# Kernel tuning notes

Hardware: AMD Instinct MI355X
Metric: run time of the kernel (lower is better)

Reference implementation:

```python
import jax, jax.numpy as jnp
import numpy as np

GROUPS = 32
EPS = 1e-5
HEADS = 8

def setup_inputs() -> dict:
    key = jax.random.key(0)
    ks = jax.random.split(key, 7)
    b, c, H, W = 16, 512, 32, 32
    x = jax.random.normal(ks[0], (b, c, H, W), dtype=jnp.float32)
    gn_scale = jax.random.normal(ks[1], (c,), dtype=jnp.float32) * 0.02 + 1.0
    gn_bias = jax.random.normal(ks[2], (c,), dtype=jnp.float32) * 0.02
    w_qkv = jax.random.normal(ks[3], (3 * c, c), dtype=jnp.float32) / np.sqrt(c)
    b_qkv = jax.random.normal(ks[4], (3 * c,), dtype=jnp.float32) * 0.01
    # original zero-initializes proj_out; use random weights for a non-trivial baseline
    w_proj = jax.random.normal(ks[5], (c, c), dtype=jnp.float32) / np.sqrt(c)
    b_proj = jax.random.normal(ks[6], (c,), dtype=jnp.float32) * 0.01
    return {"x": x, "gn_scale": gn_scale, "gn_bias": gn_bias,
            "w_qkv": w_qkv, "b_qkv": b_qkv, "w_proj": w_proj, "b_proj": b_proj}

def _group_norm(x, scale, bias):
    # x: [b, c, T]; normalize over (c//GROUPS, T) per group
    b, c, T = x.shape
    xg = x.reshape(b, GROUPS, (c // GROUPS) * T)
    mean = xg.mean(axis=-1, keepdims=True)
    var = xg.var(axis=-1, keepdims=True)
    xn = ((xg - mean) * jax.lax.rsqrt(var + EPS)).reshape(b, c, T)
    return xn * scale[None, :, None] + bias[None, :, None]

def reference(x, gn_scale, gn_bias, w_qkv, b_qkv, w_proj, b_proj):
    b, c, H, W = x.shape
    T = H * W
    xf = x.reshape(b, c, T)
    h = _group_norm(xf, gn_scale, gn_bias)
    qkv = jnp.einsum('oc,bct->bot', w_qkv, h) + b_qkv[None, :, None]  # [b, 3c, T]
    qkv = qkv.reshape(b * HEADS, 3 * (c // HEADS), T)
    ch = c // HEADS
    q, k, v = jnp.split(qkv, 3, axis=1)  # each [b*heads, ch, T]
    scale = 1.0 / np.sqrt(np.sqrt(ch))
    weight = jnp.einsum('bct,bcs->bts', q * scale, k * scale)  # [b*heads, T, T]
    weight = jax.nn.softmax(weight.astype(jnp.float32), axis=-1).astype(qkv.dtype)
    r = jnp.einsum('bts,bcs->bct', weight, v)  # [b*heads, ch, T]
    r = r.reshape(b, c, T)
    out = jnp.einsum('oc,bct->bot', w_proj, r) + b_proj[None, :, None]
    return (xf + out).reshape(b, c, H, W)
```

## Files before the change

kernel.cpp:

```cpp
#include <hip/hip_runtime.h>
#include <stdint.h>
#include <stddef.h>

#define NB 16
#define NC 512
#define NT 1024
#define NHEAD 8
#define NOC 1536

typedef float f32x4 __attribute__((ext_vector_type(4)));
typedef short s16x8 __attribute__((ext_vector_type(8)));
typedef short s16x4 __attribute__((ext_vector_type(4)));
typedef unsigned int u32x2 __attribute__((ext_vector_type(2)));

#define AS1 __attribute__((address_space(1)))
#define AS3 __attribute__((address_space(3)))

static __device__ __forceinline__ unsigned short f2bf(float f) {
  union { float fv; unsigned int u; } v; v.fv = f;
  return (unsigned short)((v.u + 0x7fffu + ((v.u >> 16) & 1u)) >> 16);
}

static __device__ __forceinline__ unsigned int cvtpk(float lo, float hi) {
  unsigned int r;
  asm("v_cvt_pk_bf16_f32 %0, %1, %2" : "=v"(r) : "v"(lo), "v"(hi));
  return r;
}

static __device__ __forceinline__ float exp2_hw(float x) {
  float r;
  asm("v_exp_f32 %0, %1" : "=v"(r) : "v"(x));
  return r;
}

__global__ void k_convert(const float* __restrict__ wq, const float* __restrict__ wp,
                          unsigned short* __restrict__ wqb, unsigned short* __restrict__ wpb) {
  int i = blockIdx.x * 256 + threadIdx.x;
  int step = gridDim.x * 256;
  for (int idx = i; idx < NOC * NC; idx += step) wqb[idx] = f2bf(wq[idx]);
  for (int idx = i; idx < NC * NC; idx += step) wpb[idx] = f2bf(wp[idx]);
}

__global__ __launch_bounds__(256) void k_gnstats(const float* __restrict__ x,
    const float* __restrict__ gsc, const float* __restrict__ gbi,
    float* __restrict__ affA, float* __restrict__ affB) {
  int b = blockIdx.x >> 5, g = blockIdx.x & 31;
  const f32x4* p4 = (const f32x4*)(x + (size_t)(b * NC + g * 16) * NT);
  float s = 0.f, ss = 0.f;
  for (int i = threadIdx.x; i < 4096; i += 256) {
    f32x4 v = p4[i];
    s += v[0] + v[1] + v[2] + v[3];
    ss += v[0] * v[0] + v[1] * v[1] + v[2] * v[2] + v[3] * v[3];
  }
#pragma unroll
  for (int off = 32; off > 0; off >>= 1) { s += __shfl_down(s, off); ss += __shfl_down(ss, off); }
  __shared__ float red[4][2];
  if ((threadIdx.x & 63) == 0) { red[threadIdx.x >> 6][0] = s; red[threadIdx.x >> 6][1] = ss; }
  __syncthreads();
  if (threadIdx.x < 16) {
    float st = red[0][0] + red[1][0] + red[2][0] + red[3][0];
    float sst = red[0][1] + red[1][1] + red[2][1] + red[3][1];
    float mean = st * (1.f / 16384.f);
    float var = sst * (1.f / 16384.f) - mean * mean;
    float rstd = rsqrtf(var + 1e-5f);
    int c = g * 16 + threadIdx.x;
    float a = rstd * gsc[c];
    affA[b * NC + c] = a;
    affB[b * NC + c] = gbi[c] - mean * a;
  }
}

__global__ __launch_bounds__(256) void k_norm_t(const float* __restrict__ x,
    const float* __restrict__ affA, const float* __restrict__ affB,
    unsigned short* __restrict__ xt) {
  __shared__ float sm[64][65];
  int bx = blockIdx.x;
  int tt = bx & 15, ct = (bx >> 4) & 7, b = bx >> 7;
  int c0 = ct * 64, t0 = tt * 64;
  int tid = threadIdx.x;
#pragma unroll
  for (int it = 0; it < 4; it++) {
    int row = (tid >> 4) + it * 16;
    int col = (tid & 15) * 4;
    int c = c0 + row;
    f32x4 v = *(const f32x4*)(x + (size_t)(b * NC + c) * NT + t0 + col);
    float a = affA[b * NC + c], bb = affB[b * NC + c];
    sm[row][col + 0] = v[0] * a + bb;
    sm[row][col + 1] = v[1] * a + bb;
    sm[row][col + 2] = v[2] * a + bb;
    sm[row][col + 3] = v[3] * a + bb;
  }
  __syncthreads();
#pragma unroll
  for (int it = 0; it < 2; it++) {
    int t = (tid >> 3) + it * 32;
    int cb = (tid & 7) * 8;
    s16x8 o;
#pragma unroll
    for (int j = 0; j < 8; j++) o[j] = (short)f2bf(sm[cb + j][t]);
    *(s16x8*)(xt + (size_t)(b * NT + t0 + t) * NC + c0 + cb) = o;
  }
}

__global__ __launch_bounds__(256) void k_qkv(const unsigned short* __restrict__ wqb,
    const unsigned short* __restrict__ xt, const float* __restrict__ bqkv,
    unsigned short* __restrict__ qt, unsigned short* __restrict__ ktb,
    unsigned short* __restrict__ vvb) {
  __shared__ char LB[32768];
  int n0 = blockIdx.x * 128;
  int m0 = blockIdx.y * 128;
  int b = blockIdx.z;
  int tid = threadIdx.x, lane = tid & 63, wid = tid >> 6;
  int wr = wid >> 1, wc = wid & 1;
  int arow = lane >> 2, acol = (lane & 3) * 8;
  f32x4 acc[4][4] = {};
#pragma unroll
  for (int cc = 0; cc < 2; cc++) {
    int ci = wid * 2 + cc;
    const unsigned short* ga = wqb + (size_t)(m0 + ci * 16 + arow) * NC + acol;
    __builtin_amdgcn_global_load_lds((const AS1 unsigned int*)ga,
                                     (AS3 unsigned int*)(LB + ci * 1024), 16, 0, 0);
    const unsigned short* gb = xt + (size_t)(b * NT + n0 + ci * 16 + arow) * NC + acol;
    __builtin_amdgcn_global_load_lds((const AS1 unsigned int*)gb,
                                     (AS3 unsigned int*)(LB + 8192 + ci * 1024), 16, 0, 0);
  }
  for (int ks = 0; ks < 16; ks++) {
    int cur = ks & 1;
    char* Ac = LB + cur * 16384;
    char* Bc = Ac + 8192;
    if (ks < 15) {
      int k0n = (ks + 1) * 32;
      char* An = LB + (cur ^ 1) * 16384;
#pragma unroll
      for (int cc = 0; cc < 2; cc++) {
        int ci = wid * 2 + cc;
        const unsigned short* ga = wqb + (size_t)(m0 + ci * 16 + arow) * NC + k0n + acol;
        __builtin_amdgcn_global_load_lds((const AS1 unsigned int*)ga,
                                         (AS3 unsigned int*)(An + ci * 1024), 16, 0, 0);
        const unsigned short* gb = xt + (size_t)(b * NT + n0 + ci * 16 + arow) * NC + k0n + acol;
        __builtin_amdgcn_global_load_lds((const AS1 unsigned int*)gb,
                                         (AS3 unsigned int*)(An + 8192 + ci * 1024), 16, 0, 0);
      }
      asm volatile("s_waitcnt vmcnt(4)" ::: "memory");
    } else {
      asm volatile("s_waitcnt vmcnt(0)" ::: "memory");
    }
    __builtin_amdgcn_s_barrier();
    __builtin_amdgcn_sched_barrier(0);
    s16x8 af[4], bfv[4];
#pragma unroll
    for (int mi = 0; mi < 4; mi++)
      af[mi] = *(const s16x8*)(Ac + ((wr * 64 + mi * 16 + (lane & 15)) * 32 + (lane >> 4) * 8) * 2);
#pragma unroll
    for (int ni = 0; ni < 4; ni++)
      bfv[ni] = *(const s16x8*)(Bc + ((wc * 64 + ni * 16 + (lane & 15)) * 32 + (lane >> 4) * 8) * 2);
#pragma unroll
    for (int mi = 0; mi < 4; mi++)
#pragma unroll
      for (int ni = 0; ni < 4; ni++)
        acc[mi][ni] = __builtin_amdgcn_mfma_f32_16x16x32_bf16(af[mi], bfv[ni], acc[mi][ni], 0, 0, 0);
    __builtin_amdgcn_s_barrier();
  }
  char* tr = LB + wid * 8192;
  int o064 = m0 + wr * 64;
  int blk = (o064 >> 6) % 3;
  int head = o064 / 192;
  int bh = b * NHEAD + head;
  int n0w = n0 + wc * 64;
  const float scale = 0.42466090014400953f;
  if (blk < 2) {
#pragma unroll
    for (int mi = 0; mi < 4; mi++) {
      int o_loc = mi * 16 + (lane >> 4) * 4;
      float b0 = bqkv[o064 + o_loc + 0], b1 = bqkv[o064 + o_loc + 1];
      float b2 = bqkv[o064 + o_loc + 2], b3 = bqkv[o064 + o_loc + 3];
#pragma unroll
      for (int ni = 0; ni < 4; ni++) {
        int t_loc = ni * 16 + (lane & 15);
        s16x4 pk;
        pk[0] = (short)f2bf((acc[mi][ni][0] + b0) * scale);
        pk[1] = (short)f2bf((acc[mi][ni][1] + b1) * scale);
        pk[2] = (short)f2bf((acc[mi][ni][2] + b2) * scale);
        pk[3] = (short)f2bf((acc[mi][ni][3] + b3) * scale);
        *(s16x4*)(tr + t_loc * 128 + ((o_loc * 2) ^ ((t_loc & 7) << 4))) = pk;
      }
    }
    unsigned short* outp = (blk == 0) ? qt : ktb;
#pragma unroll
    for (int pass = 0; pass < 8; pass++) {
      int t = pass * 8 + (lane >> 3);
      int cb = (lane & 7) * 16;
      s16x8 v = *(const s16x8*)(tr + t * 128 + (cb ^ ((t & 7) << 4)));
      *(s16x8*)(outp + (size_t)(bh * NT + n0w + t) * 64 + (cb >> 1)) = v;
    }
  } else {
#pragma unroll
    for (int mi = 0; mi < 4; mi++) {
#pragma unroll
      for (int ni = 0; ni < 4; ni++) {
        int t_loc = ni * 16 + (lane & 15);
#pragma unroll
        for (int r = 0; r < 4; r++) {
          int o_loc = mi * 16 + (lane >> 4) * 4 + r;
          *(unsigned short*)(tr + o_loc * 128 + t_loc * 2) =
              f2bf(acc[mi][ni][r] + bqkv[o064 + o_loc]);
        }
      }
    }
#pragma unroll
    for (int pass = 0; pass < 8; pass++) {
      int o = pass * 8 + (lane >> 3);
      int tb = (lane & 7) * 16;
      s16x8 v = *(const s16x8*)(tr + o * 128 + tb);
      *(s16x8*)(vvb + (size_t)(bh * 64 + o) * NT + n0w + (tb >> 1)) = v;
    }
  }
}

__global__ __launch_bounds__(512, 4) void k_attn(const unsigned short* __restrict__ qt,
    const unsigned short* __restrict__ ktb, const unsigned short* __restrict__ vvb,
    unsigned short* __restrict__ rt) {
  __shared__ char Kl[2][8192];
  __shared__ char Vl[2][8192];
  __shared__ char Pl[8][4096];
  int qt0 = blockIdx.x * 256;
  int bh = blockIdx.y;
  int b = bh >> 3, head = bh & 7;
  int tid = threadIdx.x, lane = tid & 63, wid = tid >> 6;
  int hi = lane >> 4, lo = lane & 15;
  int q0 = qt0 + wid * 32;
  s16x8 aq[2][2];
#pragma unroll
  for (int mi = 0; mi < 2; mi++)
#pragma unroll
    for (int ko = 0; ko < 2; ko++)
      aq[mi][ko] = *(const s16x8*)(qt + (size_t)(bh * NT + q0 + mi * 16 + lo) * 64 +
                                   ko * 32 + hi * 8);
  f32x4 oacc[2][4] = {};
  f32x4 lacc[2] = {};
  float mrun[2] = {-1e30f, -1e30f};
  s16x8 ones;
#pragma unroll
  for (int j = 0; j < 8; j++) ones[j] = (short)0x3F80;
  char* pl = (char*)Pl[wid];
  int srow = (wid << 3) + (lane >> 3);
  int soff = ((lane & 7) << 4) ^ ((srow & 7) << 4);
  const char* kb = (const char*)ktb + ((size_t)bh * NT + srow) * 128 + soff;
  const char* vb = (const char*)vvb + ((size_t)(bh * 64 + srow)) * 2048 + soff;
  __builtin_amdgcn_global_load_lds((const AS1 unsigned int*)kb,
                                   (AS3 unsigned int*)(Kl[0] + (wid << 10)), 16, 0, 0);
  __builtin_amdgcn_global_load_lds((const AS1 unsigned int*)vb,
                                   (AS3 unsigned int*)(Vl[0] + (wid << 10)), 16, 0, 0);
  for (int kv = 0; kv < 16; kv++) {
    int cur = kv & 1;
    if (kv < 15) {
      __builtin_amdgcn_global_load_lds((const AS1 unsigned int*)(kb + (size_t)(kv + 1) * 8192),
                                       (AS3 unsigned int*)(Kl[cur ^ 1] + (wid << 10)), 16, 0, 0);
      __builtin_amdgcn_global_load_lds((const AS1 unsigned int*)(vb + (size_t)(kv + 1) * 128),
                                       (AS3 unsigned int*)(Vl[cur ^ 1] + (wid << 10)), 16, 0, 0);
      asm volatile("s_waitcnt vmcnt(2)" ::: "memory");
    } else {
      asm volatile("s_waitcnt vmcnt(0)" ::: "memory");
    }
    __builtin_amdgcn_s_barrier();
    __builtin_amdgcn_sched_barrier(0);
    f32x4 sc[2][4] = {};
#pragma unroll
    for (int ni = 0; ni < 4; ni++) {
      int tkr = ni * 16 + lo;
#pragma unroll
      for (int ko = 0; ko < 2; ko++) {
        s16x8 kf = *(const s16x8*)(Kl[cur] + tkr * 128 + ((ko * 64 + hi * 16) ^ ((tkr & 7) << 4)));
        sc[0][ni] = __builtin_amdgcn_mfma_f32_16x16x32_bf16(kf, aq[0][ko], sc[0][ni], 0, 0, 0);
        sc[1][ni] = __builtin_amdgcn_mfma_f32_16x16x32_bf16(kf, aq[1][ko], sc[1][ni], 0, 0, 0);
      }
    }
#pragma unroll
    for (int mi = 0; mi < 2; mi++) {
      float a0 = fmaxf(fmaxf(sc[mi][0][0], sc[mi][0][1]), fmaxf(sc[mi][0][2], sc[mi][0][3]));
      float a1 = fmaxf(fmaxf(sc[mi][1][0], sc[mi][1][1]), fmaxf(sc[mi][1][2], sc[mi][1][3]));
      float a2 = fmaxf(fmaxf(sc[mi][2][0], sc[mi][2][1]), fmaxf(sc[mi][2][2], sc[mi][2][3]));
      float a3 = fmaxf(fmaxf(sc[mi][3][0], sc[mi][3][1]), fmaxf(sc[mi][3][2], sc[mi][3][3]));
      float tm = fmaxf(fmaxf(a0, a1), fmaxf(a2, a3));
      tm = fmaxf(tm, __shfl_xor(tm, 16));
      tm = fmaxf(tm, __shfl_xor(tm, 32));
      int resc = __any(tm > mrun[mi] + 8.f);
      float mnew = mrun[mi];
      if (resc) {
        mnew = fmaxf(mrun[mi], tm);
        float fac = exp2_hw(mrun[mi] - mnew);
        mrun[mi] = mnew;
#pragma unroll
        for (int dm = 0; dm < 4; dm++)
#pragma unroll
          for (int r = 0; r < 4; r++) oacc[mi][dm][r] *= fac;
#pragma unroll
        for (int r = 0; r < 4; r++) lacc[mi][r] *= fac;
      }
#pragma unroll
      for (int ni = 0; ni < 4; ni++)
#pragma unroll
        for (int r = 0; r < 4; r++) sc[mi][ni][r] = exp2_hw(sc[mi][ni][r] - mnew);
      int qrow = mi * 16 + lo;
#pragma unroll
      for (int ni = 0; ni < 4; ni++) {
        u32x2 w;
        w[0] = cvtpk(sc[mi][ni][0], sc[mi][ni][1]);
        w[1] = cvtpk(sc[mi][ni][2], sc[mi][ni][3]);
        *(u32x2*)(pl + (qrow * 128 + ((ni * 32 + hi * 8) ^ ((qrow & 7) << 4)))) = w;
      }
    }
#pragma unroll
    for (int kt = 0; kt < 2; kt++) {
      s16x8 pa[2];
#pragma unroll
      for (int mi = 0; mi < 2; mi++) {
        int qrow = mi * 16 + lo;
        pa[mi] = *(const s16x8*)(pl + (qrow * 128 + ((kt * 64 + hi * 16) ^ ((qrow & 7) << 4))));
      }
#pragma unroll
      for (int dm = 0; dm < 4; dm++) {
        int dr = dm * 16 + lo;
        s16x8 av = *(const s16x8*)(Vl[cur] + dr * 128 + ((kt * 64 + hi * 16) ^ ((dr & 7) << 4)));
        oacc[0][dm] = __builtin_amdgcn_mfma_f32_16x16x32_bf16(av, pa[0], oacc[0][dm], 0, 0, 0);
        oacc[1][dm] = __builtin_amdgcn_mfma_f32_16x16x32_bf16(av, pa[1], oacc[1][dm], 0, 0, 0);
      }
      lacc[0] = __builtin_amdgcn_mfma_f32_16x16x32_bf16(ones, pa[0], lacc[0], 0, 0, 0);
      lacc[1] = __builtin_amdgcn_mfma_f32_16x16x32_bf16(ones, pa[1], lacc[1], 0, 0, 0);
    }
    __builtin_amdgcn_s_barrier();
  }
#pragma unroll
  for (int mi = 0; mi < 2; mi++) {
    float inv = 1.f / lacc[mi][0];
    int q = q0 + mi * 16 + lo;
#pragma unroll
    for (int dm = 0; dm < 4; dm++) {
      u32x2 w;
      w[0] = cvtpk(oacc[mi][dm][0] * inv, oacc[mi][dm][1] * inv);
      w[1] = cvtpk(oacc[mi][dm][2] * inv, oacc[mi][dm][3] * inv);
      *(u32x2*)(rt + (size_t)(b * NT + q) * NC + head * 64 + dm * 16 + hi * 4) = w;
    }
  }
}

__global__ __launch_bounds__(256) void k_proj(const unsigned short* __restrict__ wpb,
    const unsigned short* __restrict__ rt, const float* __restrict__ bproj,
    const float* __restrict__ x, float* __restrict__ out) {
  __shared__ char LB[32768];
  int n0 = blockIdx.x * 128;
  int m0 = blockIdx.y * 128;
  int b = blockIdx.z;
  int tid = threadIdx.x, lane = tid & 63, wid = tid >> 6;
  int wr = wid >> 1, wc = wid & 1;
  int arow = lane >> 2, acol = (lane & 3) * 8;
  f32x4 acc[4][4] = {};
#pragma unroll
  for (int cc = 0; cc < 2; cc++) {
    int ci = wid * 2 + cc;
    const unsigned short* ga = wpb + (size_t)(m0 + ci * 16 + arow) * NC + acol;
    __builtin_amdgcn_global_load_lds((const AS1 unsigned int*)ga,
                                     (AS3 unsigned int*)(LB + ci * 1024), 16, 0, 0);
    const unsigned short* gb = rt + (size_t)(b * NT + n0 + ci * 16 + arow) * NC + acol;
    __builtin_amdgcn_global_load_lds((const AS1 unsigned int*)gb,
                                     (AS3 unsigned int*)(LB + 8192 + ci * 1024), 16, 0, 0);
  }
  for (int ks = 0; ks < 16; ks++) {
    int cur = ks & 1;
    char* Ac = LB + cur * 16384;
    char* Bc = Ac + 8192;
    if (ks < 15) {
      int k0n = (ks + 1) * 32;
      char* An = LB + (cur ^ 1) * 16384;
#pragma unroll
      for (int cc = 0; cc < 2; cc++) {
        int ci = wid * 2 + cc;
        const unsigned short* ga = wpb + (size_t)(m0 + ci * 16 + arow) * NC + k0n + acol;
        __builtin_amdgcn_global_load_lds((const AS1 unsigned int*)ga,
                                         (AS3 unsigned int*)(An + ci * 1024), 16, 0, 0);
        const unsigned short* gb = rt + (size_t)(b * NT + n0 + ci * 16 + arow) * NC + k0n + acol;
        __builtin_amdgcn_global_load_lds((const AS1 unsigned int*)gb,
                                         (AS3 unsigned int*)(An + 8192 + ci * 1024), 16, 0, 0);
      }
      asm volatile("s_waitcnt vmcnt(4)" ::: "memory");
    } else {
      asm volatile("s_waitcnt vmcnt(0)" ::: "memory");
    }
    __builtin_amdgcn_s_barrier();
    __builtin_amdgcn_sched_barrier(0);
    s16x8 af[4], bfv[4];
#pragma unroll
    for (int mi = 0; mi < 4; mi++)
      af[mi] = *(const s16x8*)(Ac + ((wr * 64 + mi * 16 + (lane & 15)) * 32 + (lane >> 4) * 8) * 2);
#pragma unroll
    for (int ni = 0; ni < 4; ni++)
      bfv[ni] = *(const s16x8*)(Bc + ((wc * 64 + ni * 16 + (lane & 15)) * 32 + (lane >> 4) * 8) * 2);
#pragma unroll
    for (int mi = 0; mi < 4; mi++)
#pragma unroll
      for (int ni = 0; ni < 4; ni++)
        acc[mi][ni] = __builtin_amdgcn_mfma_f32_16x16x32_bf16(af[mi], bfv[ni], acc[mi][ni], 0, 0, 0);
    __builtin_amdgcn_s_barrier();
  }
#pragma unroll
  for (int mi = 0; mi < 4; mi++) {
    int o_base = m0 + wr * 64 + mi * 16 + (lane >> 4) * 4;
#pragma unroll
    for (int r = 0; r < 4; r++) {
      int o = o_base + r;
      float bp = bproj[o];
#pragma unroll
      for (int ni = 0; ni < 4; ni++) {
        int t = n0 + wc * 64 + ni * 16 + (lane & 15);
        size_t idx = (size_t)(b * NC + o) * NT + t;
        out[idx] = acc[mi][ni][r] + bp + x[idx];
      }
    }
  }
}

extern "C" void kernel_launch(void* const* d_in, const int* in_sizes, int n_in,
                              void* d_out, int out_size, void* d_ws, size_t ws_size,
                              hipStream_t stream) {
  const float* x   = (const float*)d_in[0];
  const float* gsc = (const float*)d_in[1];
  const float* gbi = (const float*)d_in[2];
  const float* wq  = (const float*)d_in[3];
  const float* bq  = (const float*)d_in[4];
  const float* wp  = (const float*)d_in[5];
  const float* bp  = (const float*)d_in[6];
  float* out = (float*)d_out;
  char* ws = (char*)d_ws;

  float* affA = (float*)ws;
  float* affB = affA + NB * NC;
  unsigned short* wqb = (unsigned short*)(ws + 65536);
  unsigned short* wpb = wqb + (size_t)NOC * NC;
  unsigned short* xt  = (unsigned short*)(ws + 2162688);
  unsigned short* qt  = xt + (size_t)NB * NT * NC;
  unsigned short* ktb = qt + (size_t)128 * NT * 64;
  unsigned short* vvb = ktb + (size_t)128 * NT * 64;
  unsigned short* rt  = vvb + (size_t)128 * NT * 64;

  k_convert<<<dim3(1024), 256, 0, stream>>>(wq, wp, wqb, wpb);
  k_gnstats<<<dim3(512), 256, 0, stream>>>(x, gsc, gbi, affA, affB);
  k_norm_t<<<dim3(2048), 256, 0, stream>>>(x, affA, affB, xt);
  k_qkv<<<dim3(8, 12, 16), 256, 0, stream>>>(wqb, xt, bq, qt, ktb, vvb);
  k_attn<<<dim3(4, 128), 512, 0, stream>>>(qt, ktb, vvb, rt);
  k_proj<<<dim3(8, 4, 16), 256, 0, stream>>>(wpb, rt, bp, x, out);
}
```

Measured before the change: 127.7 us.

## Triple-buffer LDS tiles and drop trailing barrier in GEMM and attention loops

Switches the K-loop staging in the QKV, attention and projection kernels from double to triple buffering, prefetching two tiles ahead. The prefetch is now issued after the barrier, so the trailing per-iteration barrier can be removed and each iteration needs only one sync. This adds LDS per block, which may lower how many GEMM blocks fit on a CU.

```diff
diff --git a/kernel.cpp b/kernel.cpp
--- a/kernel.cpp
+++ b/kernel.cpp
@@ -106,7 +106,7 @@
     const unsigned short* __restrict__ xt, const float* __restrict__ bqkv,
     unsigned short* __restrict__ qt, unsigned short* __restrict__ ktb,
     unsigned short* __restrict__ vvb) {
-  __shared__ char LB[32768];
+  __shared__ char LB[49152];
   int n0 = blockIdx.x * 128;
   int m0 = blockIdx.y * 128;
   int b = blockIdx.z;
@@ -115,22 +115,31 @@
   int arow = lane >> 2, acol = (lane & 3) * 8;
   f32x4 acc[4][4] = {};
 #pragma unroll
-  for (int cc = 0; cc < 2; cc++) {
-    int ci = wid * 2 + cc;
-    const unsigned short* ga = wqb + (size_t)(m0 + ci * 16 + arow) * NC + acol;
-    __builtin_amdgcn_global_load_lds((const AS1 unsigned int*)ga,
-                                     (AS3 unsigned int*)(LB + ci * 1024), 16, 0, 0);
-    const unsigned short* gb = xt + (size_t)(b * NT + n0 + ci * 16 + arow) * NC + acol;
-    __builtin_amdgcn_global_load_lds((const AS1 unsigned int*)gb,
-                                     (AS3 unsigned int*)(LB + 8192 + ci * 1024), 16, 0, 0);
+  for (int t0 = 0; t0 < 2; t0++) {
+#pragma unroll
+    for (int cc = 0; cc < 2; cc++) {
+      int ci = wid * 2 + cc;
+      const unsigned short* ga = wqb + (size_t)(m0 + ci * 16 + arow) * NC + t0 * 32 + acol;
+      __builtin_amdgcn_global_load_lds((const AS1 unsigned int*)ga,
+                                       (AS3 unsigned int*)(LB + t0 * 16384 + ci * 1024), 16, 0, 0);
+      const unsigned short* gb = xt + (size_t)(b * NT + n0 + ci * 16 + arow) * NC + t0 * 32 + acol;
+      __builtin_amdgcn_global_load_lds((const AS1 unsigned int*)gb,
+                                       (AS3 unsigned int*)(LB + t0 * 16384 + 8192 + ci * 1024), 16, 0, 0);
+    }
   }
   for (int ks = 0; ks < 16; ks++) {
-    int cur = ks & 1;
-    char* Ac = LB + cur * 16384;
+    char* Ac = LB + (ks % 3) * 16384;
     char* Bc = Ac + 8192;
-    if (ks < 15) {
-      int k0n = (ks + 1) * 32;
-      char* An = LB + (cur ^ 1) * 16384;
+    if (ks < 14) {
+      asm volatile("s_waitcnt vmcnt(4)" ::: "memory");
+    } else {
+      asm volatile("s_waitcnt vmcnt(0)" ::: "memory");
+    }
+    __builtin_amdgcn_s_barrier();
+    __builtin_amdgcn_sched_barrier(0);
+    if (ks + 2 < 16) {
+      int k0n = (ks + 2) * 32;
+      char* An = LB + ((ks + 2) % 3) * 16384;
 #pragma unroll
       for (int cc = 0; cc < 2; cc++) {
         int ci = wid * 2 + cc;
@@ -141,12 +150,7 @@
         __builtin_amdgcn_global_load_lds((const AS1 unsigned int*)gb,
                                          (AS3 unsigned int*)(An + 8192 + ci * 1024), 16, 0, 0);
       }
-      asm volatile("s_waitcnt vmcnt(4)" ::: "memory");
-    } else {
-      asm volatile("s_waitcnt vmcnt(0)" ::: "memory");
-    }
-    __builtin_amdgcn_s_barrier();
-    __builtin_amdgcn_sched_barrier(0);
+    }
     s16x8 af[4], bfv[4];
 #pragma unroll
     for (int mi = 0; mi < 4; mi++)
@@ -159,8 +163,8 @@
 #pragma unroll
       for (int ni = 0; ni < 4; ni++)
         acc[mi][ni] = __builtin_amdgcn_mfma_f32_16x16x32_bf16(af[mi], bfv[ni], acc[mi][ni], 0, 0, 0);
-    __builtin_amdgcn_s_barrier();
-  }
+  }
+  __syncthreads();
   char* tr = LB + wid * 8192;
   int o064 = m0 + wr * 64;
   int blk = (o064 >> 6) % 3;
@@ -220,8 +224,8 @@
 __global__ __launch_bounds__(512, 4) void k_attn(const unsigned short* __restrict__ qt,
     const unsigned short* __restrict__ ktb, const unsigned short* __restrict__ vvb,
     unsigned short* __restrict__ rt) {
-  __shared__ char Kl[2][8192];
-  __shared__ char Vl[2][8192];
+  __shared__ char Kl[3][8192];
+  __shared__ char Vl[3][8192];
   __shared__ char Pl[8][4096];
   int qt0 = blockIdx.x * 256;
   int bh = blockIdx.y;
@@ -247,23 +251,29 @@
   int soff = ((lane & 7) << 4) ^ ((srow & 7) << 4);
   const char* kb = (const char*)ktb + ((size_t)bh * NT + srow) * 128 + soff;
   const char* vb = (const char*)vvb + ((size_t)(bh * 64 + srow)) * 2048 + soff;
-  __builtin_amdgcn_global_load_lds((const AS1 unsigned int*)kb,
-                                   (AS3 unsigned int*)(Kl[0] + (wid << 10)), 16, 0, 0);
-  __builtin_amdgcn_global_load_lds((const AS1 unsigned int*)vb,
-                                   (AS3 unsigned int*)(Vl[0] + (wid << 10)), 16, 0, 0);
+#pragma unroll
+  for (int t0 = 0; t0 < 2; t0++) {
+    __builtin_amdgcn_global_load_lds((const AS1 unsigned int*)(kb + (size_t)t0 * 8192),
+                                     (AS3 unsigned int*)(Kl[t0] + (wid << 10)), 16, 0, 0);
+    __builtin_amdgcn_global_load_lds((const AS1 unsigned int*)(vb + (size_t)t0 * 128),
+                                     (AS3 unsigned int*)(Vl[t0] + (wid << 10)), 16, 0, 0);
+  }
   for (int kv = 0; kv < 16; kv++) {
-    int cur = kv & 1;
-    if (kv < 15) {
-      __builtin_amdgcn_global_load_lds((const AS1 unsigned int*)(kb + (size_t)(kv + 1) * 8192),
-                                       (AS3 unsigned int*)(Kl[cur ^ 1] + (wid << 10)), 16, 0, 0);
-      __builtin_amdgcn_global_load_lds((const AS1 unsigned int*)(vb + (size_t)(kv + 1) * 128),
-                                       (AS3 unsigned int*)(Vl[cur ^ 1] + (wid << 10)), 16, 0, 0);
+    int cur = kv % 3;
+    if (kv < 14) {
       asm volatile("s_waitcnt vmcnt(2)" ::: "memory");
     } else {
       asm volatile("s_waitcnt vmcnt(0)" ::: "memory");
     }
     __builtin_amdgcn_s_barrier();
     __builtin_amdgcn_sched_barrier(0);
+    if (kv + 2 < 16) {
+      int nb = (kv + 2) % 3;
+      __builtin_amdgcn_global_load_lds((const AS1 unsigned int*)(kb + (size_t)(kv + 2) * 8192),
+                                       (AS3 unsigned int*)(Kl[nb] + (wid << 10)), 16, 0, 0);
+      __builtin_amdgcn_global_load_lds((const AS1 unsigned int*)(vb + (size_t)(kv + 2) * 128),
+                                       (AS3 unsigned int*)(Vl[nb] + (wid << 10)), 16, 0, 0);
+    }
     f32x4 sc[2][4] = {};
 #pragma unroll
     for (int ni = 0; ni < 4; ni++) {
@@ -328,7 +338,6 @@
       lacc[0] = __builtin_amdgcn_mfma_f32_16x16x32_bf16(ones, pa[0], lacc[0], 0, 0, 0);
       lacc[1] = __builtin_amdgcn_mfma_f32_16x16x32_bf16(ones, pa[1], lacc[1], 0, 0, 0);
     }
-    __builtin_amdgcn_s_barrier();
   }
 #pragma unroll
   for (int mi = 0; mi < 2; mi++) {
@@ -347,7 +356,7 @@
 __global__ __launch_bounds__(256) void k_proj(const unsigned short* __restrict__ wpb,
     const unsigned short* __restrict__ rt, const float* __restrict__ bproj,
     const float* __restrict__ x, float* __restrict__ out) {
-  __shared__ char LB[32768];
+  __shared__ char LB[49152];
   int n0 = blockIdx.x * 128;
   int m0 = blockIdx.y * 128;
   int b = blockIdx.z;
@@ -356,22 +365,31 @@
   int arow = lane >> 2, acol = (lane & 3) * 8;
   f32x4 acc[4][4] = {};
 #pragma unroll
-  for (int cc = 0; cc < 2; cc++) {
-    int ci = wid * 2 + cc;
-    const unsigned short* ga = wpb + (size_t)(m0 + ci * 16 + arow) * NC + acol;
-    __builtin_amdgcn_global_load_lds((const AS1 unsigned int*)ga,
-                                     (AS3 unsigned int*)(LB + ci * 1024), 16, 0, 0);
-    const unsigned short* gb = rt + (size_t)(b * NT + n0 + ci * 16 + arow) * NC + acol;
-    __builtin_amdgcn_global_load_lds((const AS1 unsigned int*)gb,
-                                     (AS3 unsigned int*)(LB + 8192 + ci * 1024), 16, 0, 0);
+  for (int t0 = 0; t0 < 2; t0++) {
+#pragma unroll
+    for (int cc = 0; cc < 2; cc++) {
+      int ci = wid * 2 + cc;
+      const unsigned short* ga = wpb + (size_t)(m0 + ci * 16 + arow) * NC + t0 * 32 + acol;
+      __builtin_amdgcn_global_load_lds((const AS1 unsigned int*)ga,
+                                       (AS3 unsigned int*)(LB + t0 * 16384 + ci * 1024), 16, 0, 0);
+      const unsigned short* gb = rt + (size_t)(b * NT + n0 + ci * 16 + arow) * NC + t0 * 32 + acol;
+      __builtin_amdgcn_global_load_lds((const AS1 unsigned int*)gb,
+                                       (AS3 unsigned int*)(LB + t0 * 16384 + 8192 + ci * 1024), 16, 0, 0);
+    }
   }
   for (int ks = 0; ks < 16; ks++) {
-    int cur = ks & 1;
-    char* Ac = LB + cur * 16384;
+    char* Ac = LB + (ks % 3) * 16384;
     char* Bc = Ac + 8192;
-    if (ks < 15) {
-      int k0n = (ks + 1) * 32;
-      char* An = LB + (cur ^ 1) * 16384;
+    if (ks < 14) {
+      asm volatile("s_waitcnt vmcnt(4)" ::: "memory");
+    } else {
+      asm volatile("s_waitcnt vmcnt(0)" ::: "memory");
+    }
+    __builtin_amdgcn_s_barrier();
+    __builtin_amdgcn_sched_barrier(0);
+    if (ks + 2 < 16) {
+      int k0n = (ks + 2) * 32;
+      char* An = LB + ((ks + 2) % 3) * 16384;
 #pragma unroll
       for (int cc = 0; cc < 2; cc++) {
         int ci = wid * 2 + cc;
@@ -382,12 +400,7 @@
         __builtin_amdgcn_global_load_lds((const AS1 unsigned int*)gb,
                                          (AS3 unsigned int*)(An + 8192 + ci * 1024), 16, 0, 0);
       }
-      asm volatile("s_waitcnt vmcnt(4)" ::: "memory");
-    } else {
-      asm volatile("s_waitcnt vmcnt(0)" ::: "memory");
-    }
-    __builtin_amdgcn_s_barrier();
-    __builtin_amdgcn_sched_barrier(0);
+    }
     s16x8 af[4], bfv[4];
 #pragma unroll
     for (int mi = 0; mi < 4; mi++)
@@ -400,7 +413,6 @@
 #pragma unroll
       for (int ni = 0; ni < 4; ni++)
         acc[mi][ni] = __builtin_amdgcn_mfma_f32_16x16x32_bf16(af[mi], bfv[ni], acc[mi][ni], 0, 0, 0);
-    __builtin_amdgcn_s_barrier();
   }
 #pragma unroll
   for (int mi = 0; mi < 4; mi++) {
```

After: 128.8 us. About the same (+0.8%).
